# Kernel optimization log

Hardware: AMD Instinct MI355X
Metric: run time of the kernel (lower is better)

Reference implementation:

```python
import jax, jax.numpy as jnp
import numpy as np

B = 128        # graphs per batch
N = 512        # nodes per graph (all graphs full-size)
F = 128        # input/hidden feature dim
DEG_AVG = 16   # average degree
E = B * N * DEG_AVG
DEGREES = (3, 3)  # polynomial filter order per conv layer


def setup_inputs() -> dict:
    key = jax.random.key(0)
    ks = jax.random.split(key, 8)
    X = jax.random.normal(ks[0], (B * N, F), dtype=jnp.float32)
    batch = jnp.repeat(jnp.arange(B, dtype=jnp.int32), N)
    # edges constrained within each graph: graph id = e // (N*DEG_AVG)
    gid = jnp.repeat(jnp.arange(B, dtype=jnp.int32), N * DEG_AVG)
    src = jax.random.randint(ks[1], (E,), 0, N, dtype=jnp.int32) + gid * N
    dst = jax.random.randint(ks[2], (E,), 0, N, dtype=jnp.int32) + gid * N
    edge_index = jnp.stack([src, dst], axis=0)
    s = 1.0 / np.sqrt(F)
    W1 = jax.random.normal(ks[3], (F, F), dtype=jnp.float32) * s
    b1 = jnp.zeros((F,), dtype=jnp.float32)
    W2 = jax.random.normal(ks[4], (F, F), dtype=jnp.float32) * s
    b2 = jnp.zeros((F,), dtype=jnp.float32)
    Wr1 = jax.random.normal(ks[5], (F, 64), dtype=jnp.float32) * s
    br1 = jnp.zeros((64,), dtype=jnp.float32)
    Wr2 = jax.random.normal(ks[6], (64, 1), dtype=jnp.float32) * (1.0 / 8.0)
    br2 = jnp.zeros((1,), dtype=jnp.float32)
    return {"X": X, "batch": batch, "edge_index": edge_index,
            "W1": W1, "b1": b1, "W2": W2, "b2": b2,
            "Wr1": Wr1, "br1": br1, "Wr2": Wr2, "br2": br2}


def _build_gso(edge_index):
    # dense per-graph adjacency [B, N, N] (block-diagonal global GSO,
    # represented batched for efficiency)
    g = edge_index[0] // N
    si = edge_index[0] % N
    di = edge_index[1] % N
    A = jnp.zeros((B, N, N), dtype=jnp.float32).at[g, si, di].set(1.0)
    # gso_generator: symmetric degree-normalized adjacency D^-1/2 A D^-1/2
    deg = A.sum(axis=-1)
    dinv = jnp.where(deg > 0, jax.lax.rsqrt(jnp.maximum(deg, 1e-12)), 0.0)
    S = dinv[:, :, None] * A * dinv[:, None, :]
    return S


def _poly_conv(S, x, degree, W, b):
    # sum_{k=0..degree} S^k x, then linear projection
    acc = x
    z = x
    for _ in range(degree):
        z = jnp.einsum('bij,bjf->bif', S, z)
        acc = acc + z
    return jnp.einsum('bnf,fo->bno', acc, W) + b


def reference(X, batch, edge_index, W1, b1, W2, b2, Wr1, br1, Wr2, br2):
    S = _build_gso(edge_index)
    x = X.reshape(B, N, F)  # nodes grouped per graph (batch is sorted)
    x = jax.nn.relu(_poly_conv(S, x, DEGREES[0], W1, b1))
    x = jax.nn.relu(_poly_conv(S, x, DEGREES[1], W2, b2))
    # global mean pool over nodes of each graph
    h = x.mean(axis=1)  # [B, F]
    h = jax.nn.relu(h @ Wr1 + br1)
    out = (h @ Wr2 + br2).squeeze(-1)  # [B]
    return out
```

## Files before the change

### kernel.cpp

```cpp
#include <hip/hip_runtime.h>
#include <hip/hip_bf16.h>

#define NB 128
#define NN 512
#define NF 128
#define BN (NB*NN)
#define NE (BN*16)
#define EPG 8192
#define WPR 16
#define ELLW 64
#define QST 32
#define SST 72
#define WTS 136

typedef short sh8 __attribute__((ext_vector_type(8)));
typedef float f32x4 __attribute__((ext_vector_type(4)));

static __device__ __forceinline__ unsigned short f2bf(float f) {
    unsigned u = __float_as_uint(f);
    u += 0x7fffu + ((u >> 16) & 1u);
    return (unsigned short)(u >> 16);
}

#define DOT2LO(acc_, pk_, one_) \
    asm("v_dot2_f32_bf16 %0, %1, %2, %0" : "+v"(acc_) : "v"(pk_), "v"(one_))

__global__ __launch_bounds__(1024) void build_ell_fused_kernel(
    const int* __restrict__ src, const int* __restrict__ dst,
    unsigned short* __restrict__ ell, int* __restrict__ ocnt,
    float* __restrict__ dinvr, int* __restrict__ perm)
{
    __shared__ unsigned bm[NN * WPR];
    __shared__ int cs[NN];
    __shared__ int rdeg[NN];
    __shared__ int irank[NN];
    __shared__ int half1[NN];
    __shared__ int half2[NN];
    __shared__ int prk[NN];
    int g = blockIdx.x;
    int t = threadIdx.x;
    int row = t & 511;
    int hb  = t >> 9;
    int wo  = hb * 8;

    for (int i = t; i < NN * WPR; i += 1024) bm[i] = 0u;
    __syncthreads();

    const int4* sg4 = (const int4*)(src + (size_t)g * EPG);
    const int4* dg4 = (const int4*)(dst + (size_t)g * EPG);
    for (int i = t; i < EPG / 4; i += 1024) {
        int4 s4 = sg4[i];
        int4 d4 = dg4[i];
        int s, d;
        s = s4.x & (NN - 1); d = d4.x & (NN - 1);
        atomicOr(&bm[s * WPR + (d >> 5)], 1u << (d & 31));
        s = s4.y & (NN - 1); d = d4.y & (NN - 1);
        atomicOr(&bm[s * WPR + (d >> 5)], 1u << (d & 31));
        s = s4.z & (NN - 1); d = d4.z & (NN - 1);
        atomicOr(&bm[s * WPR + (d >> 5)], 1u << (d & 31));
        s = s4.w & (NN - 1); d = d4.w & (NN - 1);
        atomicOr(&bm[s * WPR + (d >> 5)], 1u << (d & 31));
    }
    __syncthreads();

    unsigned rw[8];
    #pragma unroll
    for (int w = 0; w < 8; ++w) rw[w] = bm[row * WPR + wo + w];
    int pc = 0;
    #pragma unroll
    for (int w = 0; w < 8; ++w) pc += __popc(rw[w]);
    if (hb) half2[row] = pc; else half1[row] = pc;
    __syncthreads();

    if (!hb) {
        int d0 = pc + half2[row];
        if (d0 > ELLW) d0 = ELLW;
        cs[row] = d0;
    }
    __syncthreads();

    int deg_r = cs[row];
    {
        const int4* c4 = (const int4*)cs;
        int ib = hb * 64;
        int pcnt = 0;
        #pragma unroll 8
        for (int ii = 0; ii < 64; ++ii) {
            int4 v = c4[ib + ii];
            int i0 = (ib + ii) * 4;
            pcnt += (v.x < deg_r) || (v.x == deg_r && (i0 + 0) < row);
            pcnt += (v.y < deg_r) || (v.y == deg_r && (i0 + 1) < row);
            pcnt += (v.z < deg_r) || (v.z == deg_r && (i0 + 2) < row);
            pcnt += (v.w < deg_r) || (v.w == deg_r && (i0 + 3) < row);
        }
        if (!hb) prk[row] = pcnt;
        __syncthreads();
        if (hb) {
            int rk = prk[row] + pcnt;
            irank[row] = rk;
            rdeg[rk] = deg_r;
            perm[(size_t)g * NN + rk] = row;
            dinvr[(size_t)g * NN + rk] =
                (deg_r > 0) ? rsqrtf((float)deg_r) : 0.0f;
        }
    }
    __syncthreads();

    if (t < NN / 8) {
        int m = rdeg[t * 8 + 7];
        ocnt[(size_t)g * (NN / 8) + t] = (m + 3) & ~3;
    }

    unsigned short* els = (unsigned short*)bm;
    int rk = irank[row];
    for (int qtr = 0; qtr < 4; ++qtr) {
        if ((rk >> 7) == qtr) {
            unsigned short* er = &els[(rk & 127) * SST];
            int c = hb ? half1[row] : 0;
            #pragma unroll
            for (int w = 0; w < 8; ++w) {
                unsigned bits = rw[w];
                while (bits) {
                    int j = __ffs(bits) - 1;
                    bits &= bits - 1;
                    if (c < ELLW) er[c] = (unsigned short)irank[(wo + w) * 32 + j];
                    ++c;
                }
            }
            if (hb) {
                if (c > ELLW) c = ELLW;
                for (int p = c; p < ELLW; ++p) er[p] = (unsigned short)NN;
            }
        }
        __syncthreads();
        unsigned short* outb = ell + ((size_t)g * NN + qtr * 128) * ELLW;
        {
            int r2 = t >> 3, sg2 = t & 7;
            uint4 v = *(const uint4*)&els[r2 * SST + sg2 * 8];
            *(uint4*)&outb[(size_t)r2 * ELLW + sg2 * 8] = v;
        }
        __syncthreads();
    }
}

__global__ __launch_bounds__(512, 4) void poly_fused_kernel(
    const float* __restrict__ xin,
    unsigned short* __restrict__ accout,
    const unsigned short* __restrict__ ell,
    const int* __restrict__ ocnt,
    const float* __restrict__ dinvr,
    const int* __restrict__ perm,
    int permuteIn)
{
    extern __shared__ float lds[];
    unsigned short* w = (unsigned short*)lds;
    float* dsh = lds + ((NN + 1) * QST * 2) / 4;

    int b = blockIdx.x;
    int g = b & 127;
    int q = b >> 7;
    int t = threadIdx.x;
    int wid = t >> 6;
    int qd  = (t >> 2) & 15;
    int fbq = t & 3;

    unsigned one_lo = 0x00003F80u;
    unsigned one_hi = 0x3F800000u;

    if (t < NN) dsh[t] = dinvr[(size_t)g * NN + t];
    if (t < QST) w[NN * QST + t] = 0;

    int rnk[4];
    #pragma unroll
    for (int x = 0; x < 4; ++x) {
        int wl = (x >= 2) ? (7 - wid) : wid;
        rnk[x] = x * 128 + wl * 16 + qd;
    }

    const int* oc = ocnt + (size_t)g * (NN / 8);
    int co[4];
    #pragma unroll
    for (int x = 0; x < 4; ++x) {
        int ob = (rnk[x] - qd) >> 3;
        co[x] = __builtin_amdgcn_readfirstlane(max(oc[ob], oc[ob + 1]));
    }

    int px[4];
    if (permuteIn) {
        const int* pmg = perm + (size_t)g * NN;
        #pragma unroll
        for (int x = 0; x < 4; ++x) px[x] = pmg[rnk[x]];
    } else {
        #pragma unroll
        for (int x = 0; x < 4; ++x) px[x] = rnk[x];
    }

    const float* xg = xin + (size_t)g * NN * NF + q * 32 + fbq * 8;

    float acc[4][8];
    #pragma unroll
    for (int x = 0; x < 4; ++x) {
        int row = px[x];
        float4 a0 = *(const float4*)&xg[(size_t)row * NF];
        float4 a1 = *(const float4*)&xg[(size_t)row * NF + 4];
        acc[x][0] = a0.x; acc[x][1] = a0.y; acc[x][2] = a0.z; acc[x][3] = a0.w;
        acc[x][4] = a1.x; acc[x][5] = a1.y; acc[x][6] = a1.z; acc[x][7] = a1.w;
    }

    __syncthreads();

    #pragma unroll
    for (int x = 0; x < 4; ++x) {
        float di = dsh[rnk[x]];
        unsigned pk[4];
        #pragma unroll
        for (int k = 0; k < 4; ++k) {
            unsigned lo = (unsigned)f2bf(di * acc[x][2 * k]);
            unsigned hi = (unsigned)f2bf(di * acc[x][2 * k + 1]);
            pk[k] = lo | (hi << 16);
        }
        *(uint4*)&w[rnk[x] * QST + fbq * 8] = make_uint4(pk[0], pk[1], pk[2], pk[3]);
    }
    __syncthreads();

    for (int hop = 0; hop < 3; ++hop) {
        unsigned pst[4][4];
        #pragma unroll
        for (int x = 0; x < 4; ++x) {
            const unsigned short* el =
                ell + ((size_t)g * NN + rnk[x]) * ELLW;
            int cnt = co[x];
            float s[8];
            #pragma unroll
            for (int k = 0; k < 8; ++k) s[k] = 0.0f;

            ushort4 cur = *(const ushort4*)el;
            for (int p = 0; p < cnt; p += 4) {
                ushort4 nxt = cur;
                if (p + 4 < cnt) nxt = *(const ushort4*)(el + p + 4);
                uint4 v0 = *(const uint4*)&w[(int)cur.x * QST + fbq * 8];
                uint4 v1 = *(const uint4*)&w[(int)cur.y * QST + fbq * 8];
                uint4 v2 = *(const uint4*)&w[(int)cur.z * QST + fbq * 8];
                uint4 v3 = *(const uint4*)&w[(int)cur.w * QST + fbq * 8];
                unsigned d[4][4] = {{v0.x, v0.y, v0.z, v0.w},
                                    {v1.x, v1.y, v1.z, v1.w},
                                    {v2.x, v2.y, v2.z, v2.w},
                                    {v3.x, v3.y, v3.z, v3.w}};
                #pragma unroll
                for (int n = 0; n < 4; ++n) {
                    #pragma unroll
                    for (int k = 0; k < 4; ++k) {
                        DOT2LO(s[2 * k],     d[n][k], one_lo);
                        DOT2LO(s[2 * k + 1], d[n][k], one_hi);
                    }
                }
                cur = nxt;
            }

            float di = dsh[rnk[x]];
            #pragma unroll
            for (int k = 0; k < 4; ++k) {
                float zlo = di * s[2 * k];
                float zhi = di * s[2 * k + 1];
                acc[x][2 * k]     += zlo;
                acc[x][2 * k + 1] += zhi;
                unsigned lo = (unsigned)f2bf(di * zlo);
                unsigned hi = (unsigned)f2bf(di * zhi);
                pst[x][k] = lo | (hi << 16);
            }
        }
        __syncthreads();
        #pragma unroll
        for (int x = 0; x < 4; ++x) {
            *(uint4*)&w[rnk[x] * QST + fbq * 8] =
                make_uint4(pst[x][0], pst[x][1], pst[x][2], pst[x][3]);
        }
        __syncthreads();
    }

    unsigned short* og = accout + (size_t)g * NN * NF + q * 32 + fbq * 8;
    #pragma unroll
    for (int x = 0; x < 4; ++x) {
        int rr = rnk[x];
        uint4 pk;
        pk.x = (unsigned)f2bf(acc[x][0]) | ((unsigned)f2bf(acc[x][1]) << 16);
        pk.y = (unsigned)f2bf(acc[x][2]) | ((unsigned)f2bf(acc[x][3]) << 16);
        pk.z = (unsigned)f2bf(acc[x][4]) | ((unsigned)f2bf(acc[x][5]) << 16);
        pk.w = (unsigned)f2bf(acc[x][6]) | ((unsigned)f2bf(acc[x][7]) << 16);
        *(uint4*)&og[(size_t)rr * NF] = pk;
    }
}

__global__ __launch_bounds__(256, 2) void gemm_bias_relu_kernel(
    const unsigned short* __restrict__ X,
    const float* __restrict__ W,
    const float* __restrict__ b, float* __restrict__ Y,
    float* __restrict__ partial, int fuse)
{
    __shared__ __align__(16) unsigned short Wt[NF * WTS];
    __shared__ float part[4 * NF];

    int t = threadIdx.x;

    for (int i = t; i < NF * NF / 4; i += 256) {
        int k = i >> 5;
        int n4 = (i & 31) * 4;
        float4 wv = ((const float4*)W)[i];
        Wt[(n4 + 0) * WTS + k] = f2bf(wv.x);
        Wt[(n4 + 1) * WTS + k] = f2bf(wv.y);
        Wt[(n4 + 2) * WTS + k] = f2bf(wv.z);
        Wt[(n4 + 3) * WTS + k] = f2bf(wv.w);
    }
    __syncthreads();

    int lane = t & 63;
    int wid  = t >> 6;
    int quad = lane >> 4;
    int l16  = lane & 15;
    int rowA0 = blockIdx.x * 128 + wid * 32;

    union { uint4 q; sh8 v; } af[2][4];
    #pragma unroll
    for (int m = 0; m < 2; ++m) {
        int r = rowA0 + m * 16 + l16;
        const unsigned short* xr = X + (size_t)r * NF + quad * 8;
        #pragma unroll
        for (int kk = 0; kk < 4; ++kk)
            af[m][kk].q = *(const uint4*)(xr + kk * 32);
    }

    f32x4 acc[2][8];
    #pragma unroll
    for (int m = 0; m < 2; ++m)
        #pragma unroll
        for (int c = 0; c < 8; ++c) acc[m][c] = (f32x4){0.f, 0.f, 0.f, 0.f};

    #pragma unroll
    for (int c = 0; c < 8; ++c) {
        const unsigned short* wb = &Wt[(c * 16 + l16) * WTS + quad * 8];
        #pragma unroll
        for (int kk = 0; kk < 4; ++kk) {
            union { uint4 q; sh8 v; } bf_;
            bf_.q = *(const uint4*)(wb + kk * 32);
            acc[0][c] = __builtin_amdgcn_mfma_f32_16x16x32_bf16(
                af[0][kk].v, bf_.v, acc[0][c], 0, 0, 0);
            acc[1][c] = __builtin_amdgcn_mfma_f32_16x16x32_bf16(
                af[1][kk].v, bf_.v, acc[1][c], 0, 0, 0);
        }
    }

    float psum[8];
    #pragma unroll
    for (int c = 0; c < 8; ++c) psum[c] = 0.0f;

    #pragma unroll
    for (int c = 0; c < 8; ++c) {
        int col = c * 16 + l16;
        float bias = b[col];
        #pragma unroll
        for (int m = 0; m < 2; ++m) {
            #pragma unroll
            for (int reg = 0; reg < 4; ++reg) {
                int r = rowA0 + m * 16 + quad * 4 + reg;
                float v = fmaxf(acc[m][c][reg] + bias, 0.0f);
                if (!fuse) Y[(size_t)r * NF + col] = v;
                psum[c] += v;
            }
        }
    }

    if (fuse) {
        #pragma unroll
        for (int c = 0; c < 8; ++c) {
            float v = psum[c];
            v += __shfl_xor(v, 16);
            v += __shfl_xor(v, 32);
            if (lane < 16) part[wid * NF + c * 16 + lane] = v;
        }
        __syncthreads();
        if (t < NF) {
            float s = part[t] + part[NF + t] + part[2 * NF + t]
                    + part[3 * NF + t];
            partial[(size_t)blockIdx.x * NF + t] = s;
        }
    }
}

__global__ __launch_bounds__(128) void readout_kernel(
    const float* __restrict__ partial,
    const float* __restrict__ Wr1, const float* __restrict__ br1,
    const float* __restrict__ Wr2, const float* __restrict__ br2,
    float* __restrict__ out)
{
    __shared__ float hsh[NF];
    __shared__ float r1[64];

    int g = blockIdx.x;
    int t = threadIdx.x;

    const float* pg = partial + (size_t)g * 4 * NF;
    float s = 0.0f;
    #pragma unroll
    for (int j = 0; j < 4; ++j) s += pg[j * NF + t];
    hsh[t] = s * (1.0f / (float)NN);
    __syncthreads();

    if (t < 64) {
        float a = br1[t];
        #pragma unroll 8
        for (int k = 0; k < NF; ++k) a += hsh[k] * Wr1[k * 64 + t];
        r1[t] = fmaxf(a, 0.0f);
    }
    __syncthreads();

    if (t < 64) {
        float v = r1[t] * Wr2[t];
        #pragma unroll
        for (int off = 32; off; off >>= 1) v += __shfl_down(v, off);
        if (t == 0) out[g] = v + br2[0];
    }
}

extern "C" void kernel_launch(void* const* d_in, const int* in_sizes, int n_in,
                              void* d_out, int out_size, void* d_ws, size_t ws_size,
                              hipStream_t stream)
{
    const float* X    = (const float*)d_in[0];
    const int*   ei   = (const int*)d_in[2];
    const float* W1   = (const float*)d_in[3];
    const float* b1   = (const float*)d_in[4];
    const float* W2   = (const float*)d_in[5];
    const float* b2   = (const float*)d_in[6];
    const float* Wr1  = (const float*)d_in[7];
    const float* br1  = (const float*)d_in[8];
    const float* Wr2  = (const float*)d_in[9];
    const float* br2  = (const float*)d_in[10];
    float* out = (float*)d_out;

    const int* src = ei;
    const int* dst = ei + NE;

    char* ws = (char*)d_ws;
    float*          dinvr   = (float*)(ws);
    int*            ocnt    = (int*)(ws + (size_t)256 * 1024);
    int*            perm    = (int*)(ws + (size_t)512 * 1024);
    float*          partial = (float*)(ws + (size_t)768 * 1024);
    unsigned short* ell     = (unsigned short*)(ws + (size_t)1024 * 1024);
    unsigned short* buf0    = (unsigned short*)(ws + (size_t)16384 * 1024);
    float*          buf1    = (float*)(ws + (size_t)49152 * 1024);

    build_ell_fused_kernel<<<NB, 1024, 0, stream>>>(src, dst, ell, ocnt, dinvr,
                                                    perm);

    const size_t LDSSZ = (size_t)(NN + 1) * QST * 2 + NN * 4;

    poly_fused_kernel<<<NB * 4, 512, LDSSZ, stream>>>(X, buf0, ell, ocnt,
                                                      dinvr, perm, 1);
    gemm_bias_relu_kernel<<<BN / 128, 256, 0, stream>>>(buf0, W1, b1, buf1,
                                                        partial, 0);

    poly_fused_kernel<<<NB * 4, 512, LDSSZ, stream>>>(buf1, buf0, ell, ocnt,
                                                      dinvr, perm, 0);
    gemm_bias_relu_kernel<<<BN / 128, 256, 0, stream>>>(buf0, W2, b2, buf1,
                                                        partial, 1);

    readout_kernel<<<NB, 128, 0, stream>>>(partial, Wr1, br1, Wr2, br2, out);
}
```

Baseline: 222.7 us.

## Split ELL build into parallel bitmap scatter and rank/ELL kernels

Replaces the single 128-block ELL build kernel with two kernels. The first scatters edges into a per-graph adjacency bitmap across 512 blocks, each owning a quarter of the source rows, and writes the bitmap to global memory. The second reads the bitmap, computes ranks, and builds the whole ELL table in LDS in one pass instead of four quarter passes. The aim is more parallelism for the atomic scatter phase. The cost is an extra launch, a global bitmap round trip, and each scatter block reading all of its graph's edges.

```diff
diff --git a/kernel.cpp b/kernel.cpp
--- a/kernel.cpp
+++ b/kernel.cpp
@@ -25,12 +25,49 @@
 #define DOT2LO(acc_, pk_, one_) \
     asm("v_dot2_f32_bf16 %0, %1, %2, %0" : "+v"(acc_) : "v"(pk_), "v"(one_))
 
-__global__ __launch_bounds__(1024) void build_ell_fused_kernel(
+__global__ __launch_bounds__(256) void scatter_bitmap_kernel(
     const int* __restrict__ src, const int* __restrict__ dst,
+    unsigned* __restrict__ bmg)
+{
+    __shared__ unsigned bm[128 * WPR];
+    int b = blockIdx.x;
+    int g = b >> 2;
+    int qr = b & 3;
+    int t = threadIdx.x;
+
+    for (int i = t; i < 128 * WPR; i += 256) bm[i] = 0u;
+    __syncthreads();
+
+    const int4* sg4 = (const int4*)(src + (size_t)g * EPG);
+    const int4* dg4 = (const int4*)(dst + (size_t)g * EPG);
+    int lo = qr << 7;
+    for (int i = t; i < EPG / 4; i += 256) {
+        int4 s4 = sg4[i];
+        int4 d4 = dg4[i];
+        int s, d;
+        s = s4.x & (NN - 1); d = d4.x & (NN - 1);
+        if ((s >> 7) == qr) atomicOr(&bm[(s - lo) * WPR + (d >> 5)], 1u << (d & 31));
+        s = s4.y & (NN - 1); d = d4.y & (NN - 1);
+        if ((s >> 7) == qr) atomicOr(&bm[(s - lo) * WPR + (d >> 5)], 1u << (d & 31));
+        s = s4.z & (NN - 1); d = d4.z & (NN - 1);
+        if ((s >> 7) == qr) atomicOr(&bm[(s - lo) * WPR + (d >> 5)], 1u << (d & 31));
+        s = s4.w & (NN - 1); d = d4.w & (NN - 1);
+        if ((s >> 7) == qr) atomicOr(&bm[(s - lo) * WPR + (d >> 5)], 1u << (d & 31));
+    }
+    __syncthreads();
+
+    unsigned* outg = bmg + ((size_t)g * NN + (size_t)qr * 128) * WPR;
+    #pragma unroll
+    for (int i = t; i < 128 * WPR / 4; i += 256)
+        *(uint4*)&outg[i * 4] = *(const uint4*)&bm[i * 4];
+}
+
+__global__ __launch_bounds__(1024) void rank_ell_kernel(
+    const unsigned* __restrict__ bmg,
     unsigned short* __restrict__ ell, int* __restrict__ ocnt,
     float* __restrict__ dinvr, int* __restrict__ perm)
 {
-    __shared__ unsigned bm[NN * WPR];
+    __shared__ unsigned short els[NN * SST];
     __shared__ int cs[NN];
     __shared__ int rdeg[NN];
     __shared__ int irank[NN];
@@ -43,29 +80,11 @@
     int hb  = t >> 9;
     int wo  = hb * 8;
 
-    for (int i = t; i < NN * WPR; i += 1024) bm[i] = 0u;
-    __syncthreads();
-
-    const int4* sg4 = (const int4*)(src + (size_t)g * EPG);
-    const int4* dg4 = (const int4*)(dst + (size_t)g * EPG);
-    for (int i = t; i < EPG / 4; i += 1024) {
-        int4 s4 = sg4[i];
-        int4 d4 = dg4[i];
-        int s, d;
-        s = s4.x & (NN - 1); d = d4.x & (NN - 1);
-        atomicOr(&bm[s * WPR + (d >> 5)], 1u << (d & 31));
-        s = s4.y & (NN - 1); d = d4.y & (NN - 1);
-        atomicOr(&bm[s * WPR + (d >> 5)], 1u << (d & 31));
-        s = s4.z & (NN - 1); d = d4.z & (NN - 1);
-        atomicOr(&bm[s * WPR + (d >> 5)], 1u << (d & 31));
-        s = s4.w & (NN - 1); d = d4.w & (NN - 1);
-        atomicOr(&bm[s * WPR + (d >> 5)], 1u << (d & 31));
-    }
-    __syncthreads();
-
-    unsigned rw[8];
-    #pragma unroll
-    for (int w = 0; w < 8; ++w) rw[w] = bm[row * WPR + wo + w];
+    const unsigned* bgr = bmg + ((size_t)g * NN + row) * WPR + wo;
+    uint4 q0 = *(const uint4*)bgr;
+    uint4 q1 = *(const uint4*)(bgr + 4);
+    unsigned rw[8] = {q0.x, q0.y, q0.z, q0.w, q1.x, q1.y, q1.z, q1.w};
+
     int pc = 0;
     #pragma unroll
     for (int w = 0; w < 8; ++w) pc += __popc(rw[w]);
@@ -111,35 +130,32 @@
         ocnt[(size_t)g * (NN / 8) + t] = (m + 3) & ~3;
     }
 
-    unsigned short* els = (unsigned short*)bm;
-    int rk = irank[row];
-    for (int qtr = 0; qtr < 4; ++qtr) {
-        if ((rk >> 7) == qtr) {
-            unsigned short* er = &els[(rk & 127) * SST];
-            int c = hb ? half1[row] : 0;
-            #pragma unroll
-            for (int w = 0; w < 8; ++w) {
-                unsigned bits = rw[w];
-                while (bits) {
-                    int j = __ffs(bits) - 1;
-                    bits &= bits - 1;
-                    if (c < ELLW) er[c] = (unsigned short)irank[(wo + w) * 32 + j];
-                    ++c;
-                }
+    {
+        int rk = irank[row];
+        unsigned short* er = &els[rk * SST];
+        int c = hb ? half1[row] : 0;
+        #pragma unroll
+        for (int w = 0; w < 8; ++w) {
+            unsigned bits = rw[w];
+            while (bits) {
+                int j = __ffs(bits) - 1;
+                bits &= bits - 1;
+                if (c < ELLW) er[c] = (unsigned short)irank[(wo + w) * 32 + j];
+                ++c;
             }
-            if (hb) {
-                if (c > ELLW) c = ELLW;
-                for (int p = c; p < ELLW; ++p) er[p] = (unsigned short)NN;
-            }
-        }
-        __syncthreads();
-        unsigned short* outb = ell + ((size_t)g * NN + qtr * 128) * ELLW;
-        {
-            int r2 = t >> 3, sg2 = t & 7;
-            uint4 v = *(const uint4*)&els[r2 * SST + sg2 * 8];
-            *(uint4*)&outb[(size_t)r2 * ELLW + sg2 * 8] = v;
-        }
-        __syncthreads();
+        }
+        if (hb) {
+            if (c > ELLW) c = ELLW;
+            for (int p = c; p < ELLW; ++p) er[p] = (unsigned short)NN;
+        }
+    }
+    __syncthreads();
+
+    unsigned short* outb = ell + (size_t)g * NN * ELLW;
+    for (int idx = t; idx < NN * 8; idx += 1024) {
+        int r2 = idx >> 3, sg2 = idx & 7;
+        uint4 v = *(const uint4*)&els[r2 * SST + sg2 * 8];
+        *(uint4*)&outb[(size_t)r2 * ELLW + sg2 * 8] = v;
     }
 }
 
@@ -446,11 +462,12 @@
     int*            perm    = (int*)(ws + (size_t)512 * 1024);
     float*          partial = (float*)(ws + (size_t)768 * 1024);
     unsigned short* ell     = (unsigned short*)(ws + (size_t)1024 * 1024);
+    unsigned*       bmg     = (unsigned*)(ws + (size_t)9216 * 1024);
     unsigned short* buf0    = (unsigned short*)(ws + (size_t)16384 * 1024);
     float*          buf1    = (float*)(ws + (size_t)49152 * 1024);
 
-    build_ell_fused_kernel<<<NB, 1024, 0, stream>>>(src, dst, ell, ocnt, dinvr,
-                                                    perm);
+    scatter_bitmap_kernel<<<NB * 4, 256, 0, stream>>>(src, dst, bmg);
+    rank_ell_kernel<<<NB, 1024, 0, stream>>>(bmg, ell, ocnt, dinvr, perm);
 
     const size_t LDSSZ = (size_t)(NN + 1) * QST * 2 + NN * 4;
 
```

Measured after the change: 220.3 us. No clear change (-1.1%).
